# Kernel optimization log

Hardware: AMD Instinct MI355X
Metric: run time of the kernel (lower is better)

Reference implementation:

```python
import jax, jax.numpy as jnp
import numpy as np

B, L, O, K, H = 8192, 128, 512, 8, 20  # batch, num_latent, num_obs, causes/node, hidden


def setup_inputs() -> dict:
    key = jax.random.key(0)
    ks = jax.random.split(key, 7)
    x = jax.random.normal(ks[0], (B, L), dtype=jnp.float32)
    # noise ~ Normal(0, 0.1), one scalar per (sample, observed node); noise_coeff = 1.0
    noise = 0.1 * jax.random.normal(ks[1], (B, O), dtype=jnp.float32)
    # latent-cause indices per observed node (fixed in-degree K)
    cause_idx = jax.random.randint(ks[2], (O, K), 0, L, dtype=jnp.int32)
    # per-node MLP weights: Linear(K+1,H) -> tanh -> Linear(H,H) -> tanh -> Linear(H,1)
    W1 = jax.random.normal(ks[3], (O, K + 1, H), dtype=jnp.float32) / np.sqrt(K + 1).astype(np.float32)
    b1 = jnp.zeros((O, H), dtype=jnp.float32)
    W2 = jax.random.normal(ks[4], (O, H, H), dtype=jnp.float32) / np.sqrt(H).astype(np.float32)
    b2 = jnp.zeros((O, H), dtype=jnp.float32)
    W3 = jax.random.normal(ks[5], (O, H), dtype=jnp.float32) / np.sqrt(H).astype(np.float32)
    b3 = jnp.zeros((O,), dtype=jnp.float32)
    return {"x": x, "noise": noise, "cause_idx": cause_idx,
            "W1": W1, "b1": b1, "W2": W2, "b2": b2, "W3": W3, "b3": b3}


def reference(x, noise, cause_idx, W1, b1, W2, b2, W3, b3):
    # Gather each observed node's latent causes: [B, O, K]
    gathered = x[:, cause_idx]
    # Prepend the noise column (torch.cat((noise, x_subset), axis=1)): [B, O, K+1]
    inp = jnp.concatenate([noise[..., None], gathered], axis=-1)
    # Per-node tiny MLP as grouped batched GEMMs
    h = jnp.tanh(jnp.einsum('boi,oih->boh', inp, W1) + b1)   # [B, O, H]
    h = jnp.tanh(jnp.einsum('boh,ohg->bog', h, W2) + b2)     # [B, O, H]
    out = jnp.einsum('boh,oh->bo', h, W3) + b3               # [B, O] (concat of per-node outputs)
    return out
```

## Files before the change

kernel.cpp:

```cpp
#include <hip/hip_runtime.h>

#define B_TOT 8192
#define O_DIM 512
#define L_DIM 128
#define K_DIM 8
#define H_DIM 20

#define TB 64
#define G  16
#define NW 4
#define NTH 256
#define XSTR 65
#define NSTR 17

__device__ __forceinline__ float fast_tanh(float x) {
    float e = __builtin_amdgcn_exp2f(x * 2.885390081777927f);
    float r = __builtin_amdgcn_rcpf(1.0f + e);
    return 1.0f - 2.0f * r;
}

__global__ __launch_bounds__(NTH, 4) void medil_fused(
    const float* __restrict__ x, const float* __restrict__ noise,
    const int* __restrict__ cause_idx,
    const float* __restrict__ W1, const float* __restrict__ b1,
    const float* __restrict__ W2, const float* __restrict__ b2,
    const float* __restrict__ W3, const float* __restrict__ b3,
    float* __restrict__ out)
{
    __shared__ float xT[L_DIM * XSTR];
    __shared__ float nt[TB * NSTR];

    const int tid = threadIdx.x;
    const int o0 = (blockIdx.x & 31) * G;
    const int b0 = (blockIdx.x >> 5) * TB;

    {
        const float4* xg = (const float4*)(x + (size_t)b0 * L_DIM);
        #pragma unroll
        for (int i = 0; i < 8; ++i) {
            int idx = tid + NTH * i;
            int r = idx >> 5, c4 = idx & 31;
            float4 v = xg[r * 32 + c4];
            xT[(c4 * 4 + 0) * XSTR + r] = v.x;
            xT[(c4 * 4 + 1) * XSTR + r] = v.y;
            xT[(c4 * 4 + 2) * XSTR + r] = v.z;
            xT[(c4 * 4 + 3) * XSTR + r] = v.w;
        }
    }
    {
        int r = tid >> 2, c4 = tid & 3;
        float4 v = *(const float4*)(noise + (size_t)(b0 + r) * O_DIM + o0 + c4 * 4);
        nt[r * NSTR + c4 * 4 + 0] = v.x;
        nt[r * NSTR + c4 * 4 + 1] = v.y;
        nt[r * NSTR + c4 * 4 + 2] = v.z;
        nt[r * NSTR + c4 * 4 + 3] = v.w;
    }
    __syncthreads();

    const int lane = tid & 63;
    const int wv = tid >> 6;

    #pragma unroll
    for (int it = 0; it < G / NW; ++it) {
        const int ol = __builtin_amdgcn_readfirstlane(wv * (G / NW) + it);
        const int o  = o0 + ol;

        const float* w1p = W1 + (size_t)o * (K_DIM + 1) * H_DIM;
        const float* b1p = b1 + (size_t)o * H_DIM;
        const float* w2p = W2 + (size_t)o * H_DIM * H_DIM;
        const float* b2p = b2 + (size_t)o * H_DIM;
        const float* w3p = W3 + (size_t)o * H_DIM;
        const int*   cip = cause_idx + (size_t)o * K_DIM;

        float xi[K_DIM];
        #pragma unroll
        for (int k = 0; k < K_DIM; ++k)
            xi[k] = xT[cip[k] * XSTR + lane];
        float inp0 = nt[lane * NSTR + ol];

        float a1[H_DIM];
        #pragma unroll
        for (int h = 0; h < H_DIM; ++h)
            a1[h] = fmaf(inp0, w1p[h], b1p[h]);
        #pragma unroll
        for (int k = 0; k < K_DIM; ++k)
            #pragma unroll
            for (int h = 0; h < H_DIM; ++h)
                a1[h] = fmaf(xi[k], w1p[(k + 1) * H_DIM + h], a1[h]);
        #pragma unroll
        for (int h = 0; h < H_DIM; ++h) a1[h] = fast_tanh(a1[h]);

        float a2[H_DIM];
        #pragma unroll
        for (int g = 0; g < H_DIM; ++g) a2[g] = b2p[g];
        #pragma unroll
        for (int h = 0; h < H_DIM; ++h)
            #pragma unroll
            for (int g = 0; g < H_DIM; ++g)
                a2[g] = fmaf(a1[h], w2p[h * H_DIM + g], a2[g]);
        #pragma unroll
        for (int g = 0; g < H_DIM; ++g) a2[g] = fast_tanh(a2[g]);

        float r = b3[o];
        #pragma unroll
        for (int h = 0; h < H_DIM; ++h) r = fmaf(a2[h], w3p[h], r);
        out[(size_t)(b0 + lane) * O_DIM + o] = r;
    }
}

extern "C" void kernel_launch(void* const* d_in, const int* in_sizes, int n_in,
                              void* d_out, int out_size, void* d_ws, size_t ws_size,
                              hipStream_t stream) {
    const float* x         = (const float*)d_in[0];
    const float* noise     = (const float*)d_in[1];
    const int*   cause_idx = (const int*)d_in[2];
    const float* W1        = (const float*)d_in[3];
    const float* b1        = (const float*)d_in[4];
    const float* W2        = (const float*)d_in[5];
    const float* b2        = (const float*)d_in[6];
    const float* W3        = (const float*)d_in[7];
    const float* b3        = (const float*)d_in[8];
    float* out = (float*)d_out;

    dim3 grid((B_TOT / TB) * (O_DIM / G));
    dim3 block(NTH);
    hipLaunchKernelGGL(medil_fused, grid, block, 0, stream,
                       x, noise, cause_idx, W1, b1, W2, b2, W3, b3, out);
}
```

Baseline: 192.3 us.

## Drop LDS staging, gather x from global, and compute two batch rows per thread

Removes the shared-memory transpose of x and the noise tile, along with the block barrier. Each lane now gathers its latent causes and noise directly from global memory. Each thread handles two batch rows (128 per block), so every scalar weight load is reused across two rows, and the per-node loop is no longer unrolled. The cost is strided, uncoalesced global gathers of x (row stride 512 bytes per lane) that depend on L2 hits, and higher register pressure from doubled activation arrays.

```diff
diff --git a/kernel.cpp b/kernel.cpp
--- a/kernel.cpp
+++ b/kernel.cpp
@@ -6,12 +6,11 @@
 #define K_DIM 8
 #define H_DIM 20
 
-#define TB 64
-#define G  16
-#define NW 4
+#define TO  16
+#define TBB 128
+#define RBS 2
+#define NW  4
 #define NTH 256
-#define XSTR 65
-#define NSTR 17
 
 __device__ __forceinline__ float fast_tanh(float x) {
     float e = __builtin_amdgcn_exp2f(x * 2.885390081777927f);
@@ -27,42 +26,19 @@
     const float* __restrict__ W3, const float* __restrict__ b3,
     float* __restrict__ out)
 {
-    __shared__ float xT[L_DIM * XSTR];
-    __shared__ float nt[TB * NSTR];
+    const int tid  = threadIdx.x;
+    const int lane = tid & 63;
+    const int wv   = tid >> 6;
+    const int o0 = (blockIdx.x & 31) * TO;
+    const int b0 = (blockIdx.x >> 5) * TBB;
 
-    const int tid = threadIdx.x;
-    const int o0 = (blockIdx.x & 31) * G;
-    const int b0 = (blockIdx.x >> 5) * TB;
+    int brow[RBS];
+    #pragma unroll
+    for (int r = 0; r < RBS; ++r) brow[r] = b0 + r * 64 + lane;
 
-    {
-        const float4* xg = (const float4*)(x + (size_t)b0 * L_DIM);
-        #pragma unroll
-        for (int i = 0; i < 8; ++i) {
-            int idx = tid + NTH * i;
-            int r = idx >> 5, c4 = idx & 31;
-            float4 v = xg[r * 32 + c4];
-            xT[(c4 * 4 + 0) * XSTR + r] = v.x;
-            xT[(c4 * 4 + 1) * XSTR + r] = v.y;
-            xT[(c4 * 4 + 2) * XSTR + r] = v.z;
-            xT[(c4 * 4 + 3) * XSTR + r] = v.w;
-        }
-    }
-    {
-        int r = tid >> 2, c4 = tid & 3;
-        float4 v = *(const float4*)(noise + (size_t)(b0 + r) * O_DIM + o0 + c4 * 4);
-        nt[r * NSTR + c4 * 4 + 0] = v.x;
-        nt[r * NSTR + c4 * 4 + 1] = v.y;
-        nt[r * NSTR + c4 * 4 + 2] = v.z;
-        nt[r * NSTR + c4 * 4 + 3] = v.w;
-    }
-    __syncthreads();
-
-    const int lane = tid & 63;
-    const int wv = tid >> 6;
-
-    #pragma unroll
-    for (int it = 0; it < G / NW; ++it) {
-        const int ol = __builtin_amdgcn_readfirstlane(wv * (G / NW) + it);
+    #pragma unroll 1
+    for (int it = 0; it < TO / NW; ++it) {
+        const int ol = __builtin_amdgcn_readfirstlane(wv * (TO / NW) + it);
         const int o  = o0 + ol;
 
         const float* w1p = W1 + (size_t)o * (K_DIM + 1) * H_DIM;
@@ -72,39 +48,72 @@
         const float* w3p = W3 + (size_t)o * H_DIM;
         const int*   cip = cause_idx + (size_t)o * K_DIM;
 
-        float xi[K_DIM];
+        float xi[RBS][K_DIM];
         #pragma unroll
-        for (int k = 0; k < K_DIM; ++k)
-            xi[k] = xT[cip[k] * XSTR + lane];
-        float inp0 = nt[lane * NSTR + ol];
+        for (int k = 0; k < K_DIM; ++k) {
+            const int col = cip[k];
+            #pragma unroll
+            for (int r = 0; r < RBS; ++r)
+                xi[r][k] = x[(size_t)brow[r] * L_DIM + col];
+        }
+        float inp0[RBS];
+        #pragma unroll
+        for (int r = 0; r < RBS; ++r)
+            inp0[r] = noise[(size_t)brow[r] * O_DIM + o];
 
-        float a1[H_DIM];
+        float a1[RBS][H_DIM];
         #pragma unroll
-        for (int h = 0; h < H_DIM; ++h)
-            a1[h] = fmaf(inp0, w1p[h], b1p[h]);
+        for (int h = 0; h < H_DIM; ++h) {
+            const float w = w1p[h], bb = b1p[h];
+            #pragma unroll
+            for (int r = 0; r < RBS; ++r) a1[r][h] = fmaf(inp0[r], w, bb);
+        }
         #pragma unroll
         for (int k = 0; k < K_DIM; ++k)
             #pragma unroll
-            for (int h = 0; h < H_DIM; ++h)
-                a1[h] = fmaf(xi[k], w1p[(k + 1) * H_DIM + h], a1[h]);
-        #pragma unroll
-        for (int h = 0; h < H_DIM; ++h) a1[h] = fast_tanh(a1[h]);
-
-        float a2[H_DIM];
-        #pragma unroll
-        for (int g = 0; g < H_DIM; ++g) a2[g] = b2p[g];
+            for (int h = 0; h < H_DIM; ++h) {
+                const float w = w1p[(k + 1) * H_DIM + h];
+                #pragma unroll
+                for (int r = 0; r < RBS; ++r) a1[r][h] = fmaf(xi[r][k], w, a1[r][h]);
+            }
         #pragma unroll
         for (int h = 0; h < H_DIM; ++h)
             #pragma unroll
-            for (int g = 0; g < H_DIM; ++g)
-                a2[g] = fmaf(a1[h], w2p[h * H_DIM + g], a2[g]);
+            for (int r = 0; r < RBS; ++r) a1[r][h] = fast_tanh(a1[r][h]);
+
+        float a2[RBS][H_DIM];
         #pragma unroll
-        for (int g = 0; g < H_DIM; ++g) a2[g] = fast_tanh(a2[g]);
+        for (int g = 0; g < H_DIM; ++g) {
+            const float bb = b2p[g];
+            #pragma unroll
+            for (int r = 0; r < RBS; ++r) a2[r][g] = bb;
+        }
+        #pragma unroll
+        for (int h = 0; h < H_DIM; ++h)
+            #pragma unroll
+            for (int g = 0; g < H_DIM; ++g) {
+                const float w = w2p[h * H_DIM + g];
+                #pragma unroll
+                for (int r = 0; r < RBS; ++r) a2[r][g] = fmaf(a1[r][h], w, a2[r][g]);
+            }
+        #pragma unroll
+        for (int g = 0; g < H_DIM; ++g)
+            #pragma unroll
+            for (int r = 0; r < RBS; ++r) a2[r][g] = fast_tanh(a2[r][g]);
 
-        float r = b3[o];
+        const float b3v = b3[o];
+        float res[RBS];
         #pragma unroll
-        for (int h = 0; h < H_DIM; ++h) r = fmaf(a2[h], w3p[h], r);
-        out[(size_t)(b0 + lane) * O_DIM + o] = r;
+        for (int r = 0; r < RBS; ++r) res[r] = b3v;
+        #pragma unroll
+        for (int h = 0; h < H_DIM; ++h) {
+            const float w = w3p[h];
+            #pragma unroll
+            for (int r = 0; r < RBS; ++r) res[r] = fmaf(a2[r][h], w, res[r]);
+        }
+        #pragma unroll
+        for (int r = 0; r < RBS; ++r)
+            out[(size_t)brow[r] * O_DIM + o] = res[r];
     }
 }
 
@@ -122,7 +131,7 @@
     const float* b3        = (const float*)d_in[8];
     float* out = (float*)d_out;
 
-    dim3 grid((B_TOT / TB) * (O_DIM / G));
+    dim3 grid((B_TOT / TBB) * (O_DIM / TO));
     dim3 block(NTH);
     hipLaunchKernelGGL(medil_fused, grid, block, 0, stream,
                        x, noise, cause_idx, W1, b1, W2, b2, W3, b3, out);
```

Result: slower. 223.1 us (+16.0%).
